# Performance work log

Hardware: AMD Instinct MI355X
Metric: run time of the kernel (lower is better)

Reference implementation:

```python
import jax, jax.numpy as jnp
import numpy as np
from jax import lax

V, E, H, B, T = 50000, 300, 1024, 128, 512
KEY_LEN = 15
PAD_IDX = 1


def setup_inputs() -> dict:
    key = jax.random.key(0)
    ks = jax.random.split(key, 9)
    s = 1.0 / np.sqrt(H)
    x = jax.random.randint(ks[0], (B, T), 0, V)
    key_ids = jax.random.randint(ks[1], (1, KEY_LEN), 0, V)
    emb = jax.random.normal(ks[2], (V, E), dtype=jnp.float32) * 0.1
    emb = emb.at[PAD_IDX].set(0.0)  # padding_idx row is zero
    W_ih = jax.random.uniform(ks[3], (3 * H, E), minval=-s, maxval=s, dtype=jnp.float32)
    W_hh = jax.random.uniform(ks[4], (3 * H, H), minval=-s, maxval=s, dtype=jnp.float32)
    b_ih = jax.random.uniform(ks[5], (3 * H,), minval=-s, maxval=s, dtype=jnp.float32)
    b_hh = jax.random.uniform(ks[6], (3 * H,), minval=-s, maxval=s, dtype=jnp.float32)
    W_g = jax.random.uniform(ks[7], (H, H), minval=-s, maxval=s, dtype=jnp.float32)
    b_g = jax.random.uniform(ks[8], (H,), minval=-s, maxval=s, dtype=jnp.float32)
    return {"x": x, "key_ids": key_ids, "emb": emb, "W_ih": W_ih, "W_hh": W_hh,
            "b_ih": b_ih, "b_hh": b_hh, "W_g": W_g, "b_g": b_g}


def _run_gru(xe, W_ih, W_hh, b_ih, b_hh, gate=None):
    # xe: [B, T, E] -> final hidden [B, H]; torch GRU gate convention (r, z, n)
    b, t, _ = xe.shape
    h_dim = W_hh.shape[1]
    xproj = jnp.einsum('bte,ge->btg', xe, W_ih) + b_ih  # [B, T, 3H], precomputed input GEMM

    def step(h, xp):
        hp = h @ W_hh.T + b_hh
        xr, xz, xn = jnp.split(xp, 3, axis=-1)
        hr, hz, hn = jnp.split(hp, 3, axis=-1)
        r = jax.nn.sigmoid(xr + hr)
        z = jax.nn.sigmoid(xz + hz)
        n = jnp.tanh(xn + r * hn)
        h_new = (1.0 - z) * n + z * h
        if gate is not None:
            h_new = gate * h_new  # key-conditioned gating injected each timestep
        return h_new, None

    h0 = jnp.zeros((b, h_dim), xe.dtype)
    hT, _ = lax.scan(step, h0, jnp.swapaxes(xproj, 0, 1))  # scan over time
    return hT


def reference(x, key_ids, emb, W_ih, W_hh, b_ih, b_hh, W_g, b_g):
    # KeyedGRU: run GRU over key embeddings, derive a sigmoid key gate,
    # then run the keyed recurrence over the input sequence.
    key_emb = emb[key_ids]              # [1, 15, E]
    k_h = _run_gru(key_emb, W_ih, W_hh, b_ih, b_hh)  # [1, H]
    gate = jax.nn.sigmoid(k_h @ W_g.T + b_g)          # [1, H], broadcast over batch
    xe = emb[x]                         # [B, T, E]
    out = _run_gru(xe, W_ih, W_hh, b_ih, b_hh, gate=gate)  # [B, H]
    return out
```

## Files before the change

### kernel.cpp

```cpp
#include <hip/hip_runtime.h>

#define B_   128
#define T_   512
#define E_   300
#define H_   1024
#define KL_  15
#define G3_  3072

#define NBLK 256
#define NTHR 512
#define GT   (NBLK*NTHR)
#define NWAVE_G (GT/64)

#define ASEG 352
#define NR   44

typedef __attribute__((ext_vector_type(8))) short short8;
typedef __attribute__((ext_vector_type(4))) float floatx4;

__device__ __align__(16) unsigned short g_Abuf[2][ASEG][B_][8];
__device__ float g_keyxp[KL_][G3_];
__device__ float g_kh[2][H_];
__device__ float g_gate[H_];

__device__ unsigned g_abar[NBLK * 32];
__device__ unsigned g_gen;

__device__ __forceinline__ void gbar(unsigned step) {
    const int tid = threadIdx.x, bid = blockIdx.x;
    __syncthreads();
    if (tid == 0)
        __hip_atomic_store(&g_abar[bid * 32], step, __ATOMIC_RELEASE, __HIP_MEMORY_SCOPE_AGENT);
    if (bid == 0) {
        if (tid < NBLK) {
            while (__hip_atomic_load(&g_abar[tid * 32], __ATOMIC_RELAXED, __HIP_MEMORY_SCOPE_AGENT) < step)
                __builtin_amdgcn_s_sleep(8);
        }
        __syncthreads();
        if (tid == 0)
            __hip_atomic_store(&g_gen, step, __ATOMIC_RELEASE, __HIP_MEMORY_SCOPE_AGENT);
    } else {
        if (tid == 0) {
            while (__hip_atomic_load(&g_gen, __ATOMIC_RELAXED, __HIP_MEMORY_SCOPE_AGENT) < step)
                __builtin_amdgcn_s_sleep(8);
        }
    }
    if (tid == 0)
        (void)__hip_atomic_load(&g_gen, __ATOMIC_ACQUIRE, __HIP_MEMORY_SCOPE_AGENT);
    __syncthreads();
}

__device__ __forceinline__ float sigf(float v){ return 1.0f/(1.0f+expf(-v)); }
__device__ __forceinline__ unsigned short bfhi(float f){
    unsigned u = __float_as_uint(f);
    return (unsigned short)((u + 0x7FFFu + ((u>>16)&1u)) >> 16);
}
__device__ __forceinline__ float bf2f(unsigned short h){ return __uint_as_float(((unsigned)h)<<16); }

#define GLOAD_LDS16(g, l) __builtin_amdgcn_global_load_lds( \
    (const __attribute__((address_space(1))) unsigned int*)(g), \
    (__attribute__((address_space(3))) unsigned int*)(l), 16, 0, 0)

__global__ void __launch_bounds__(NTHR, 1) keyed_gru_kernel(
    const int* __restrict__ x, const int* __restrict__ key_ids,
    const float* __restrict__ emb, const float* __restrict__ W_ih,
    const float* __restrict__ W_hh, const float* __restrict__ b_ih,
    const float* __restrict__ b_hh, const float* __restrict__ W_g,
    const float* __restrict__ b_g, float* __restrict__ out)
{
    const int tid  = threadIdx.x;
    const int bid  = blockIdx.x;
    const int gtid = bid * NTHR + tid;

    unsigned bstep = __hip_atomic_load(&g_gen, __ATOMIC_RELAXED, __HIP_MEMORY_SCOPE_AGENT);

    __shared__ __align__(16) unsigned short Blds[ASEG][16][8];
    __shared__ __align__(16) unsigned short Aring[4][8][8][16][8];
    __shared__ float hloc[B_][4];
    __shared__ float lbias[4][4];
    __shared__ float lgate[4];

    const int j0 = bid * 4;

    for (int idx = gtid; idx < 2*ASEG*B_*8; idx += GT)
        ((unsigned short*)g_Abuf)[idx] = 0;
    for (int idx = gtid; idx < B_*384; idx += GT) {
        int b = idx / 384, jj = idx % 384;
        float v = (jj < E_) ? emb[(size_t)x[b*T_ + 0]*E_ + jj] : 0.f;
        unsigned short hi = bfhi(v);
        g_Abuf[0][256 + (jj>>3)][b][jj&7] = hi;
        g_Abuf[0][304 + (jj>>3)][b][jj&7] = bfhi(v - bf2f(hi));
    }
    for (int idx = gtid; idx < KL_*G3_; idx += GT) {
        int s = idx / G3_, g = idx - s*G3_;
        const float* e = emb + (size_t)key_ids[s]*E_;
        const float* wv = W_ih + (size_t)g*E_;
        float acc = b_ih[g];
        for (int k = 0; k < E_; ++k) acc = fmaf(e[k], wv[k], acc);
        g_keyxp[s][g] = acc;
    }
    if (gtid < H_) g_kh[0][gtid] = 0.f;
    for (int idx = tid; idx < ASEG*16; idx += NTHR) {
        int seg = idx >> 4, c = idx & 15;
        unsigned short v[8];
        if (c >= 12) {
            #pragma unroll
            for (int e2 = 0; e2 < 8; ++e2) v[e2] = 0;
        } else {
            int wr = (c < 4) ? (j0 + c) : (c < 8) ? (H_ + j0 + c - 4) : (2*H_ + j0 + c - 8);
            if (seg < 128) {
                const float* src = W_hh + (size_t)wr*H_ + seg*8;
                #pragma unroll
                for (int e2 = 0; e2 < 8; ++e2) v[e2] = bfhi(src[e2]);
            } else if (seg < 256) {
                const float* src = W_hh + (size_t)wr*H_ + (seg-128)*8;
                #pragma unroll
                for (int e2 = 0; e2 < 8; ++e2) { unsigned short hi = bfhi(src[e2]); v[e2] = bfhi(src[e2] - bf2f(hi)); }
            } else if (seg < 304) {
                int k0 = (seg-256)*8;
                #pragma unroll
                for (int e2 = 0; e2 < 8; ++e2) { int k = k0+e2; v[e2] = (k < E_) ? bfhi(W_ih[(size_t)wr*E_ + k]) : (unsigned short)0; }
            } else {
                int k0 = (seg-304)*8;
                #pragma unroll
                for (int e2 = 0; e2 < 8; ++e2) {
                    int k = k0+e2;
                    if (k < E_) { float f = W_ih[(size_t)wr*E_ + k]; unsigned short hi = bfhi(f); v[e2] = bfhi(f - bf2f(hi)); }
                    else v[e2] = 0;
                }
            }
        }
        #pragma unroll
        for (int e2 = 0; e2 < 8; ++e2) Blds[seg][c][e2] = v[e2];
    }
    hloc[tid >> 2][tid & 3] = 0.f;
    gbar(++bstep);

    const int wid0 = gtid >> 6;
    const int lane = tid & 63;
    int cur = 0;
    for (int t = 0; t < KL_; ++t) {
        for (int j = wid0; j < H_; j += NWAVE_G) {
            const float* wr = W_hh + (size_t)j * H_;
            const float* wz = W_hh + (size_t)(j + H_) * H_;
            const float* wn = W_hh + (size_t)(j + 2*H_) * H_;
            float ar = 0.f, az = 0.f, an = 0.f;
            for (int k = lane; k < H_; k += 64) {
                float hv = g_kh[cur][k];
                ar = fmaf(hv, wr[k], ar); az = fmaf(hv, wz[k], az); an = fmaf(hv, wn[k], an);
            }
            #pragma unroll
            for (int off = 32; off > 0; off >>= 1) {
                ar += __shfl_down(ar, off); az += __shfl_down(az, off); an += __shfl_down(an, off);
            }
            if (lane == 0) {
                float r = sigf(g_keyxp[t][j] + ar + b_hh[j]);
                float z = sigf(g_keyxp[t][j + H_] + az + b_hh[j + H_]);
                float n = tanhf(g_keyxp[t][j + 2*H_] + r * (an + b_hh[j + 2*H_]));
                g_kh[cur ^ 1][j] = (1.f - z) * n + z * g_kh[cur][j];
            }
        }
        gbar(++bstep);
        cur ^= 1;
    }
    for (int j = wid0; j < H_; j += NWAVE_G) {
        const float* wg = W_g + (size_t)j * H_;
        float a = 0.f;
        for (int k = lane; k < H_; k += 64) a = fmaf(g_kh[cur][k], wg[k], a);
        #pragma unroll
        for (int off = 32; off > 0; off >>= 1) a += __shfl_down(a, off);
        if (lane == 0) g_gate[j] = sigf(a + b_g[j]);
    }
    gbar(++bstep);

    if (tid < 4) {
        int j = j0 + tid;
        lgate[tid]    = g_gate[j];
        lbias[tid][0] = b_ih[j] + b_hh[j];
        lbias[tid][1] = b_ih[H_+j] + b_hh[H_+j];
        lbias[tid][2] = b_hh[2*H_+j];
        lbias[tid][3] = b_ih[2*H_+j];
    }
    __syncthreads();

    const int w  = tid >> 6;
    const int ln = tid & 63;
    const int mw = w * 16;
    const int fr = ln & 15;
    const int fq = ln >> 4;

    for (int t = 0; t < T_; ++t) {
        const int par = t & 1;
        const unsigned short* Ab = &g_Abuf[par][0][0][0];

        floatx4 aH0 = {0,0,0,0}, aH1 = {0,0,0,0}, aE0 = {0,0,0,0}, aE1 = {0,0,0,0};

        #pragma unroll
        for (int pr = 0; pr < 2; ++pr) {
            GLOAD_LDS16(Ab + ((size_t)((pr*8     + (ln>>4))*128 + mw + (ln&15)))*8, &Aring[pr][w][0][0][0]);
            GLOAD_LDS16(Ab + ((size_t)((pr*8 + 4 + (ln>>4))*128 + mw + (ln&15)))*8, &Aring[pr][w][4][0][0]);
        }

        for (int r = 0; r < NR; ++r) {
            if (r < NR-2) {
                const int rr = r + 2, sl2 = rr & 3;
                GLOAD_LDS16(Ab + ((size_t)((rr*8     + (ln>>4))*128 + mw + (ln&15)))*8, &Aring[sl2][w][0][0][0]);
                GLOAD_LDS16(Ab + ((size_t)((rr*8 + 4 + (ln>>4))*128 + mw + (ln&15)))*8, &Aring[sl2][w][4][0][0]);
                asm volatile("s_waitcnt vmcnt(4)" ::: "memory");
            } else if (r == NR-2) {
                asm volatile("s_waitcnt vmcnt(2)" ::: "memory");
            } else {
                asm volatile("s_waitcnt vmcnt(0)" ::: "memory");
            }
            const int sl = r & 3;
            #pragma unroll
            for (int kk = 0; kk < 2; ++kk) {
                short8 af = *(const short8*)&Aring[sl][w][kk*4 + fq][fr][0];
                if (r < 16) {
                    const int bs = r*8 + kk*4 + fq;
                    aH0 = __builtin_amdgcn_mfma_f32_16x16x32_bf16(af, *(const short8*)&Blds[bs][fr][0], aH0, 0, 0, 0);
                    aH1 = __builtin_amdgcn_mfma_f32_16x16x32_bf16(af, *(const short8*)&Blds[128 + bs][fr][0], aH1, 0, 0, 0);
                } else if (r < 32) {
                    const int bs = (r-16)*8 + kk*4 + fq;
                    if (kk == 0) aH0 = __builtin_amdgcn_mfma_f32_16x16x32_bf16(af, *(const short8*)&Blds[bs][fr][0], aH0, 0, 0, 0);
                    else         aH1 = __builtin_amdgcn_mfma_f32_16x16x32_bf16(af, *(const short8*)&Blds[bs][fr][0], aH1, 0, 0, 0);
                } else if (r < 38) {
                    const int bs = 256 + (r-32)*8 + kk*4 + fq;
                    aE0 = __builtin_amdgcn_mfma_f32_16x16x32_bf16(af, *(const short8*)&Blds[bs][fr][0], aE0, 0, 0, 0);
                    aE1 = __builtin_amdgcn_mfma_f32_16x16x32_bf16(af, *(const short8*)&Blds[48 + bs][fr][0], aE1, 0, 0, 0);
                } else {
                    const int bs = 256 + (r-38)*8 + kk*4 + fq;
                    if (kk == 0) aE0 = __builtin_amdgcn_mfma_f32_16x16x32_bf16(af, *(const short8*)&Blds[bs][fr][0], aE0, 0, 0, 0);
                    else         aE1 = __builtin_amdgcn_mfma_f32_16x16x32_bf16(af, *(const short8*)&Blds[bs][fr][0], aE1, 0, 0, 0);
                }
            }
        }

        __syncthreads();
        float* Cex = (float*)&Aring[0][0][0][0][0];
        {
            floatx4 accH = aH0 + aH1, accE = aE0 + aE1;
            #pragma unroll
            for (int reg = 0; reg < 4; ++reg) {
                Cex[((w*2 + 0)*16 + (fq*4 + reg))*16 + fr] = accH[reg];
                Cex[((w*2 + 1)*16 + (fq*4 + reg))*16 + fr] = accE[reg];
            }
        }
        __syncthreads();
        {
            const int b = tid >> 2, jl = tid & 3;
            const int wv = b >> 4, rowl = b & 15;
            float sr = Cex[((wv*2+0)*16 + rowl)*16 + jl]     + Cex[((wv*2+1)*16 + rowl)*16 + jl];
            float sz = Cex[((wv*2+0)*16 + rowl)*16 + 4 + jl] + Cex[((wv*2+1)*16 + rowl)*16 + 4 + jl];
            float hn = Cex[((wv*2+0)*16 + rowl)*16 + 8 + jl];
            float xn = Cex[((wv*2+1)*16 + rowl)*16 + 8 + jl];
            float rg = sigf(sr + lbias[jl][0]);
            float zg = sigf(sz + lbias[jl][1]);
            float ng = tanhf(xn + lbias[jl][3] + rg * (hn + lbias[jl][2]));
            float hold = hloc[b][jl];
            float hnew = lgate[jl] * ((1.f - zg) * ng + zg * hold);
            hloc[b][jl] = hnew;
            const int j = j0 + jl;
            unsigned short hi = bfhi(hnew);
            g_Abuf[par ^ 1][j>>3][b][j&7] = hi;
            g_Abuf[par ^ 1][128 + (j>>3)][b][j&7] = bfhi(hnew - bf2f(hi));
            if (t == T_-1) out[(size_t)b*H_ + j] = hnew;
        }
        if (t + 1 < T_ && tid < 192) {
            int idx = bid * 192 + tid;
            int b2 = idx / 384, jj = idx % 384;
            float v = (jj < E_) ? emb[(size_t)x[b2*T_ + t + 1]*E_ + jj] : 0.f;
            unsigned short hi = bfhi(v);
            g_Abuf[par ^ 1][256 + (jj>>3)][b2][jj&7] = hi;
            g_Abuf[par ^ 1][304 + (jj>>3)][b2][jj&7] = bfhi(v - bf2f(hi));
        }
        gbar(++bstep);
    }
}

extern "C" void kernel_launch(void* const* d_in, const int* in_sizes, int n_in,
                              void* d_out, int out_size, void* d_ws, size_t ws_size,
                              hipStream_t stream) {
    const int*   x       = (const int*)d_in[0];
    const int*   key_ids = (const int*)d_in[1];
    const float* emb     = (const float*)d_in[2];
    const float* W_ih    = (const float*)d_in[3];
    const float* W_hh    = (const float*)d_in[4];
    const float* b_ih    = (const float*)d_in[5];
    const float* b_hh    = (const float*)d_in[6];
    const float* W_g     = (const float*)d_in[7];
    const float* b_g     = (const float*)d_in[8];
    float* out = (float*)d_out;

    void* args[] = {(void*)&x, (void*)&key_ids, (void*)&emb, (void*)&W_ih, (void*)&W_hh,
                    (void*)&b_ih, (void*)&b_hh, (void*)&W_g, (void*)&b_g, (void*)&out};
    hipLaunchCooperativeKernel((const void*)keyed_gru_kernel,
                               dim3(NBLK), dim3(NTHR), args, 0, stream);
}
```

Baseline: 18.90 ms.

## Use relaxed agent-scope stores with a lighter grid barrier and deeper A prefetch

Replaces the release/acquire grid barrier inside the per-timestep loops with a light variant that uses relaxed atomics. Cross-block visibility now comes from agent-scope relaxed stores of the shared hidden-state buffers, and the spin sleep interval is shortened. The barrier flag array is packed instead of padded per cache line. The A-operand LDS ring prefetch depth also goes from 2 to 3 stages. Relying on relaxed ordering risks memory-model correctness, and packing the flags may cause false sharing between polling blocks.

```diff
diff --git a/kernel.cpp b/kernel.cpp
--- a/kernel.cpp
+++ b/kernel.cpp
@@ -23,18 +23,18 @@
 __device__ float g_kh[2][H_];
 __device__ float g_gate[H_];
 
-__device__ unsigned g_abar[NBLK * 32];
+__device__ unsigned g_abar[NBLK];
 __device__ unsigned g_gen;
 
-__device__ __forceinline__ void gbar(unsigned step) {
+__device__ __forceinline__ void gbar_heavy(unsigned step) {
     const int tid = threadIdx.x, bid = blockIdx.x;
     __syncthreads();
     if (tid == 0)
-        __hip_atomic_store(&g_abar[bid * 32], step, __ATOMIC_RELEASE, __HIP_MEMORY_SCOPE_AGENT);
+        __hip_atomic_store(&g_abar[bid], step, __ATOMIC_RELEASE, __HIP_MEMORY_SCOPE_AGENT);
     if (bid == 0) {
         if (tid < NBLK) {
-            while (__hip_atomic_load(&g_abar[tid * 32], __ATOMIC_RELAXED, __HIP_MEMORY_SCOPE_AGENT) < step)
-                __builtin_amdgcn_s_sleep(8);
+            while (__hip_atomic_load(&g_abar[tid], __ATOMIC_RELAXED, __HIP_MEMORY_SCOPE_AGENT) < step)
+                __builtin_amdgcn_s_sleep(2);
         }
         __syncthreads();
         if (tid == 0)
@@ -42,7 +42,31 @@
     } else {
         if (tid == 0) {
             while (__hip_atomic_load(&g_gen, __ATOMIC_RELAXED, __HIP_MEMORY_SCOPE_AGENT) < step)
-                __builtin_amdgcn_s_sleep(8);
+                __builtin_amdgcn_s_sleep(2);
+        }
+    }
+    if (tid == 0)
+        (void)__hip_atomic_load(&g_gen, __ATOMIC_ACQUIRE, __HIP_MEMORY_SCOPE_AGENT);
+    __syncthreads();
+}
+
+__device__ __forceinline__ void gbar_light(unsigned step) {
+    const int tid = threadIdx.x, bid = blockIdx.x;
+    __syncthreads();
+    if (tid == 0)
+        __hip_atomic_store(&g_abar[bid], step, __ATOMIC_RELAXED, __HIP_MEMORY_SCOPE_AGENT);
+    if (bid == 0) {
+        if (tid < NBLK) {
+            while (__hip_atomic_load(&g_abar[tid], __ATOMIC_RELAXED, __HIP_MEMORY_SCOPE_AGENT) < step)
+                __builtin_amdgcn_s_sleep(2);
+        }
+        __syncthreads();
+        if (tid == 0)
+            __hip_atomic_store(&g_gen, step, __ATOMIC_RELAXED, __HIP_MEMORY_SCOPE_AGENT);
+    } else {
+        if (tid == 0) {
+            while (__hip_atomic_load(&g_gen, __ATOMIC_RELAXED, __HIP_MEMORY_SCOPE_AGENT) < step)
+                __builtin_amdgcn_s_sleep(2);
         }
     }
     if (tid == 0)
@@ -56,6 +80,13 @@
     return (unsigned short)((u + 0x7FFFu + ((u>>16)&1u)) >> 16);
 }
 __device__ __forceinline__ float bf2f(unsigned short h){ return __uint_as_float(((unsigned)h)<<16); }
+
+__device__ __forceinline__ void st_agent_u16(unsigned short* p, unsigned short v){
+    __hip_atomic_store(p, v, __ATOMIC_RELAXED, __HIP_MEMORY_SCOPE_AGENT);
+}
+__device__ __forceinline__ void st_agent_f32(float* p, float v){
+    __hip_atomic_store(p, v, __ATOMIC_RELAXED, __HIP_MEMORY_SCOPE_AGENT);
+}
 
 #define GLOAD_LDS16(g, l) __builtin_amdgcn_global_load_lds( \
     (const __attribute__((address_space(1))) unsigned int*)(g), \
@@ -134,7 +165,7 @@
         for (int e2 = 0; e2 < 8; ++e2) Blds[seg][c][e2] = v[e2];
     }
     hloc[tid >> 2][tid & 3] = 0.f;
-    gbar(++bstep);
+    gbar_heavy(++bstep);
 
     const int wid0 = gtid >> 6;
     const int lane = tid & 63;
@@ -157,10 +188,10 @@
                 float r = sigf(g_keyxp[t][j] + ar + b_hh[j]);
                 float z = sigf(g_keyxp[t][j + H_] + az + b_hh[j + H_]);
                 float n = tanhf(g_keyxp[t][j + 2*H_] + r * (an + b_hh[j + 2*H_]));
-                g_kh[cur ^ 1][j] = (1.f - z) * n + z * g_kh[cur][j];
-            }
-        }
-        gbar(++bstep);
+                st_agent_f32(&g_kh[cur ^ 1][j], (1.f - z) * n + z * g_kh[cur][j]);
+            }
+        }
+        gbar_light(++bstep);
         cur ^= 1;
     }
     for (int j = wid0; j < H_; j += NWAVE_G) {
@@ -169,9 +200,9 @@
         for (int k = lane; k < H_; k += 64) a = fmaf(g_kh[cur][k], wg[k], a);
         #pragma unroll
         for (int off = 32; off > 0; off >>= 1) a += __shfl_down(a, off);
-        if (lane == 0) g_gate[j] = sigf(a + b_g[j]);
-    }
-    gbar(++bstep);
+        if (lane == 0) st_agent_f32(&g_gate[j], sigf(a + b_g[j]));
+    }
+    gbar_light(++bstep);
 
     if (tid < 4) {
         int j = j0 + tid;
@@ -196,16 +227,18 @@
         floatx4 aH0 = {0,0,0,0}, aH1 = {0,0,0,0}, aE0 = {0,0,0,0}, aE1 = {0,0,0,0};
 
         #pragma unroll
-        for (int pr = 0; pr < 2; ++pr) {
+        for (int pr = 0; pr < 3; ++pr) {
             GLOAD_LDS16(Ab + ((size_t)((pr*8     + (ln>>4))*128 + mw + (ln&15)))*8, &Aring[pr][w][0][0][0]);
             GLOAD_LDS16(Ab + ((size_t)((pr*8 + 4 + (ln>>4))*128 + mw + (ln&15)))*8, &Aring[pr][w][4][0][0]);
         }
 
         for (int r = 0; r < NR; ++r) {
-            if (r < NR-2) {
-                const int rr = r + 2, sl2 = rr & 3;
+            if (r < NR-3) {
+                const int rr = r + 3, sl2 = rr & 3;
                 GLOAD_LDS16(Ab + ((size_t)((rr*8     + (ln>>4))*128 + mw + (ln&15)))*8, &Aring[sl2][w][0][0][0]);
                 GLOAD_LDS16(Ab + ((size_t)((rr*8 + 4 + (ln>>4))*128 + mw + (ln&15)))*8, &Aring[sl2][w][4][0][0]);
+                asm volatile("s_waitcnt vmcnt(6)" ::: "memory");
+            } else if (r == NR-3) {
                 asm volatile("s_waitcnt vmcnt(4)" ::: "memory");
             } else if (r == NR-2) {
                 asm volatile("s_waitcnt vmcnt(2)" ::: "memory");
@@ -262,19 +295,19 @@
             hloc[b][jl] = hnew;
             const int j = j0 + jl;
             unsigned short hi = bfhi(hnew);
-            g_Abuf[par ^ 1][j>>3][b][j&7] = hi;
-            g_Abuf[par ^ 1][128 + (j>>3)][b][j&7] = bfhi(hnew - bf2f(hi));
-            if (t == T_-1) out[(size_t)b*H_ + j] = hnew;
+            st_agent_u16(&g_Abuf[par ^ 1][j>>3][b][j&7], hi);
+            st_agent_u16(&g_Abuf[par ^ 1][128 + (j>>3)][b][j&7], bfhi(hnew - bf2f(hi)));
+            if (t == T_-1) st_agent_f32(&out[(size_t)b*H_ + j], hnew);
         }
         if (t + 1 < T_ && tid < 192) {
             int idx = bid * 192 + tid;
             int b2 = idx / 384, jj = idx % 384;
             float v = (jj < E_) ? emb[(size_t)x[b2*T_ + t + 1]*E_ + jj] : 0.f;
             unsigned short hi = bfhi(v);
-            g_Abuf[par ^ 1][256 + (jj>>3)][b2][jj&7] = hi;
-            g_Abuf[par ^ 1][304 + (jj>>3)][b2][jj&7] = bfhi(v - bf2f(hi));
-        }
-        gbar(++bstep);
+            st_agent_u16(&g_Abuf[par ^ 1][256 + (jj>>3)][b2][jj&7], hi);
+            st_agent_u16(&g_Abuf[par ^ 1][304 + (jj>>3)][b2][jj&7], bfhi(v - bf2f(hi)));
+        }
+        gbar_light(++bstep);
     }
 }
 
```

Measured after the change: 15.41 ms. 1.23x faster.
